# Kernel optimization log

Hardware: AMD Instinct MI355X
Metric: run time of the kernel (lower is better)

The kernel has to match this reference:

```python
import jax, jax.numpy as jnp
import numpy as np
from jax import lax

N, E, D, L = 10000, 320000, 128, 5
ATOM_V, BOND_V, WHID, CHID, P = 128, 16, 64, 20, 10
BN_EPS = 1e-5


def setup_inputs() -> dict:
    key = jax.random.key(0)
    it = iter(jax.random.split(key, 40))

    def nrm(shape, fan_in):
        return jax.random.normal(next(it), shape, jnp.float32) / np.sqrt(fan_in).astype(np.float32)

    return {
        "x_feat": jax.random.randint(next(it), (N, 2), 0, ATOM_V),
        "edge_index": jax.random.randint(next(it), (2, E), 0, N),
        "edge_attr": jax.random.randint(next(it), (E, 3), 0, BOND_V),
        "norm_edge_weight": jax.random.uniform(next(it), (E,), jnp.float32),
        "norm_self_loop": jax.random.uniform(next(it), (N,), jnp.float32),
        "atom_emb": nrm((2, ATOM_V, D), 1.0),
        "curv_w1": nrm((D, CHID), D), "curv_b1": jnp.zeros((CHID,), jnp.float32),
        "curv_w2": nrm((CHID, 1), CHID), "curv_b2": jnp.zeros((1,), jnp.float32),
        "fn_w1": nrm((D, CHID), D), "fn_b1": jnp.zeros((CHID,), jnp.float32),
        "fn_w2": nrm((CHID, 1), CHID), "fn_b2": jnp.zeros((1,), jnp.float32),
        "wm_w1": nrm((E, WHID), E), "wm_b1": jnp.zeros((WHID,), jnp.float32),
        "wm_w2": nrm((WHID, WHID), WHID), "wm_b2": jnp.zeros((WHID,), jnp.float32),
        "wm_w3": nrm((WHID, E), WHID), "wm_b3": jnp.zeros((E,), jnp.float32),
        "bond_emb": nrm((L, 3, BOND_V, D), 1.0),
        "conv_w1": nrm((L, D, D), D), "conv_b1": jnp.zeros((L, D), jnp.float32),
        "conv_bn_g": jnp.ones((L, D), jnp.float32), "conv_bn_b": jnp.zeros((L, D), jnp.float32),
        "conv_w2": nrm((L, D, D), D), "conv_b2": jnp.zeros((L, D), jnp.float32),
        "conv_eps": jnp.full((L,), 0.1, jnp.float32),
        "bn_g": jnp.ones((L, D), jnp.float32), "bn_b": jnp.zeros((L, D), jnp.float32),
        "batch": jnp.zeros((N,), jnp.int32),
    }


def _forward(x_feat, edge_index, edge_attr, norm_edge_weight, norm_self_loop,
             atom_emb, curv_w1, curv_b1, curv_w2, curv_b2,
             fn_w1, fn_b1, fn_w2, fn_b2,
             wm_w1, wm_b1, wm_w2, wm_b2, wm_w3, wm_b3,
             bond_emb, conv_w1, conv_b1, conv_bn_g, conv_bn_b, conv_w2, conv_b2,
             conv_eps, bn_g, bn_b):
    relu, sig = jax.nn.relu, jax.nn.sigmoid
    src, dst = edge_index[0], edge_index[1]

    # AtomEncoder: sum of per-column embeddings -> [N, D]
    x = atom_emb[0][x_feat[:, 0]] + atom_emb[1][x_feat[:, 1]]

    # CurvatureMLP: sigmoid(MLP(x)) -> kappa [N, 1]
    kappa = sig(relu(x @ curv_w1 + curv_b1) @ curv_w2 + curv_b2)

    # WeightMLP over 1-D edge-feature-sum vector (single sample of dim E)
    ea = edge_attr.sum(axis=1).astype(jnp.float32)  # [E]
    w = relu(ea @ wm_w1 + wm_b1)
    w = relu(w @ wm_w2 + wm_b2)
    weights = sig(w @ wm_w3 + wm_b3)  # [E]

    # curvature terms: scatter_add at SRC (as in original compute_gamma*)
    seg = lambda v: jax.ops.segment_sum(v, src, num_segments=N)
    f = sig(relu(x @ fn_w1 + fn_b1) @ fn_w2 + fn_b2)[:, 0]  # [N]
    fd = f[dst] - f[src]
    gamma = 0.5 * seg(weights * fd * fd)              # [N]
    delta_f = seg(weights * fd)                       # [N]
    delta_gamma = seg(weights * (gamma[dst] - gamma[src]))
    gfd = 0.5 * seg(weights * fd * (delta_f[dst] - delta_f[src]))
    gamma2 = 0.5 * delta_gamma - gfd                  # [N]
    # NOTE: kappa [N,1] * gamma [N] broadcasts to [N,N] (faithful to original)
    curv_loss = jnp.sum(relu(kappa * gamma - gamma2)) - jnp.sum(kappa)

    kap = kappa[:, 0]

    def bn(h, g, b):  # BatchNorm1d in training mode (batch stats, biased var)
        m = h.mean(axis=0)
        v = jnp.var(h, axis=0)
        return g * (h - m) * lax.rsqrt(v + BN_EPS) + b

    h_list = [x]
    for l in range(L):
        k = min(int(N * P * l / 100), 100)  # num vertices to suppress
        if k > 0:
            idx = lax.top_k(kap, k)[1]
            vm = jnp.ones(N, jnp.float32).at[idx].set(0.0)
            mew = jnp.where((vm[src] == 0) | (vm[dst] == 0), 1e-5, 1.0)
        else:
            mew = jnp.ones(E, jnp.float32)
        # BondEncoder for this layer
        ee = (bond_emb[l, 0][edge_attr[:, 0]]
              + bond_emb[l, 1][edge_attr[:, 1]]
              + bond_emb[l, 2][edge_attr[:, 2]])  # [E, D]
        # message: norm2 * norm * relu(x_j + edge_emb); aggregate add at dst
        msg = (mew * norm_edge_weight)[:, None] * relu(h_list[l][src] + ee)
        aggr = jax.ops.segment_sum(msg, dst, num_segments=N)
        h = conv_eps[l] * norm_self_loop[:, None] * h_list[l] + aggr
        # conv MLP: Linear -> BN -> ReLU -> Linear
        h = relu(bn(h @ conv_w1[l] + conv_b1[l], conv_bn_g[l], conv_bn_b[l])) @ conv_w2[l] + conv_b2[l]
        h = bn(h, bn_g[l], bn_b[l])
        if l < L - 1:  # dropout has ratio 0.0 -> no-op
            h = relu(h)
        h_list.append(h)

    node_rep = h_list[0]
    for h in h_list[1:]:
        node_rep = node_rep + h
    return node_rep, curv_loss


def reference(x_feat, edge_index, edge_attr, norm_edge_weight, norm_self_loop,
              atom_emb, curv_w1, curv_b1, curv_w2, curv_b2,
              fn_w1, fn_b1, fn_w2, fn_b2,
              wm_w1, wm_b1, wm_w2, wm_b2, wm_w3, wm_b3,
              bond_emb, conv_w1, conv_b1, conv_bn_g, conv_bn_b, conv_w2, conv_b2,
              conv_eps, bn_g, bn_b, batch):
    return _forward(x_feat, edge_index, edge_attr, norm_edge_weight, norm_self_loop,
                    atom_emb, curv_w1, curv_b1, curv_w2, curv_b2,
                    fn_w1, fn_b1, fn_w2, fn_b2,
                    wm_w1, wm_b1, wm_w2, wm_b2, wm_w3, wm_b3,
                    bond_emb, conv_w1, conv_b1, conv_bn_g, conv_bn_b, conv_w2, conv_b2,
                    conv_eps, bn_g, bn_b)
```

## Files before the change

### kernel.cpp

```cpp
#include <hip/hip_runtime.h>
#include <hip/hip_bf16.h>
#include <math.h>

#define N_NODES 10000
#define N_EDGES 320000
#define DIM     128
#define NLAYERS 5
#define CHIDN   20
#define BNEPS   1e-5f
#define TOPK    100

__device__ __forceinline__ float sigmoidf_(float x){ return 1.0f/(1.0f + expf(-x)); }

__global__ void k_init(int* counts, float* gamma, float* delta_f, float* dg, float* gfd,
                       double* wh_acc, double* kapsum, double* lossacc)
{
  int i = blockIdx.x*blockDim.x + threadIdx.x;
  int stride = gridDim.x*blockDim.x;
  for (int j=i; j<N_NODES; j+=stride){ counts[j]=0; gamma[j]=0.f; delta_f[j]=0.f; dg[j]=0.f; gfd[j]=0.f; }
  if (i < 64){ wh_acc[i]=0.0; kapsum[i]=0.0; lossacc[i]=0.0; }
}

__global__ __launch_bounds__(256) void k_node(
  const int* __restrict__ xf, const float* __restrict__ atom_emb,
  const float* __restrict__ cw1, const float* __restrict__ cb1,
  const float* __restrict__ cw2, const float* __restrict__ cb2,
  const float* __restrict__ fw1, const float* __restrict__ fb1,
  const float* __restrict__ fw2, const float* __restrict__ fb2,
  float* __restrict__ x_out, float* __restrict__ kap, float* __restrict__ fv,
  double* __restrict__ kapsum)
{
  __shared__ float scw1[DIM*CHIDN];
  __shared__ float sfw1[DIM*CHIDN];
  __shared__ float sx[4][DIM];
  __shared__ float sred[4][64];
  int tid = threadIdx.x;
  for (int i=tid;i<DIM*CHIDN;i+=256){ scw1[i]=cw1[i]; sfw1[i]=fw1[i]; }
  int wid = tid>>6, lane = tid&63;
  int n = blockIdx.x*4 + wid;
  const float* e0 = atom_emb;
  const float* e1 = atom_emb + 128*DIM;
  int f0 = xf[n*2+0], f1 = xf[n*2+1];
  float2 a = *(const float2*)(e0 + f0*DIM + lane*2);
  float2 b = *(const float2*)(e1 + f1*DIM + lane*2);
  float2 xv; xv.x = a.x+b.x; xv.y = a.y+b.y;
  *(float2*)(x_out + (size_t)n*DIM + lane*2) = xv;
  sx[wid][lane*2] = xv.x; sx[wid][lane*2+1] = xv.y;
  __syncthreads();
  if (lane < CHIDN) {
    float acc = cb1[lane];
    for (int d=0; d<DIM; ++d) acc = fmaf(sx[wid][d], scw1[d*CHIDN+lane], acc);
    sred[wid][lane] = fmaxf(acc, 0.f) * cw2[lane];
  } else if (lane >= 32 && lane < 32+CHIDN) {
    int hh = lane-32;
    float acc = fb1[hh];
    for (int d=0; d<DIM; ++d) acc = fmaf(sx[wid][d], sfw1[d*CHIDN+hh], acc);
    sred[wid][32+hh] = fmaxf(acc, 0.f) * fw2[hh];
  }
  __syncthreads();
  if (lane == 0) {
    float s = cb2[0];
    for (int h=0;h<CHIDN;++h) s += sred[wid][h];
    float kp = sigmoidf_(s);
    kap[n] = kp;
    sred[wid][62] = kp;
  } else if (lane == 1) {
    float s = fb2[0];
    for (int h=0;h<CHIDN;++h) s += sred[wid][32+h];
    fv[n] = sigmoidf_(s);
  }
  __syncthreads();
  if (tid == 0) {
    double ks = (double)sred[0][62] + (double)sred[1][62] + (double)sred[2][62] + (double)sred[3][62];
    atomicAdd(&kapsum[blockIdx.x & 63], ks);
  }
}

__global__ __launch_bounds__(256) void k_edge_pre(
  const int* __restrict__ ei, const int* __restrict__ eattr,
  const float* __restrict__ w1, int* __restrict__ counts, int* __restrict__ rank,
  double* __restrict__ wh_acc)
{
  __shared__ float part_[4][64];
  int tid = threadIdx.x;
  int wid = tid>>6, lane = tid&63;
  int bb = blockIdx.x*4 + wid;
  int e = bb*64 + lane;
  int a0=eattr[e*3], a1=eattr[e*3+1], a2=eattr[e*3+2];
  float ea = (float)(a0+a1+a2);
  int dst = ei[N_EDGES+e];
  rank[e] = atomicAdd(&counts[dst], 1);
  const float* wrow = w1 + (size_t)bb*64*64;
  float acc = 0.f;
  #pragma unroll 16
  for (int t=0;t<64;++t) {
    float eat = __shfl(ea, t);
    acc = fmaf(eat, wrow[t*64 + lane], acc);
  }
  part_[wid][lane] = acc;
  __syncthreads();
  if (tid < 64) {
    float s = part_[0][tid]+part_[1][tid]+part_[2][tid]+part_[3][tid];
    atomicAdd(&wh_acc[tid], (double)s);
  }
}

__global__ __launch_bounds__(1024) void k_topk_scan(
  const float* __restrict__ kap, int* __restrict__ mask,
  const int* __restrict__ counts, int* __restrict__ offs)
{
  __shared__ int sbuf[1024];
  __shared__ int hist[256];
  __shared__ unsigned s_prefix;
  __shared__ int s_krem;
  int tid = threadIdx.x;
  if (blockIdx.x == 0) {
    unsigned prefix = 0; int krem = TOPK;
    for (int pass=3; pass>=0; --pass) {
      if (tid<256) hist[tid]=0;
      __syncthreads();
      int shift = pass*8;
      unsigned hi_mask = (pass==3) ? 0u : (0xFFFFFFFFu << (shift+8));
      for (int i=tid;i<N_NODES;i+=1024) {
        unsigned b = __float_as_uint(kap[i]);
        if ((b & hi_mask) == (prefix & hi_mask))
          atomicAdd(&hist[(b>>shift)&255], 1);
      }
      __syncthreads();
      if (tid==0) {
        int c=0; int b=255;
        for (; b>0; --b){ int h=hist[b]; if (c+h >= krem) break; c+=h; }
        s_prefix = prefix | ((unsigned)b << shift);
        s_krem = krem - c;
      }
      __syncthreads();
      prefix = s_prefix; krem = s_krem;
      __syncthreads();
    }
    unsigned thr = prefix;
    const int per = 10;
    int base = tid*per;
    int cnt = 0;
    for (int i=base; i<base+per && i<N_NODES; ++i)
      if (__float_as_uint(kap[i])==thr) cnt++;
    sbuf[tid]=cnt; __syncthreads();
    for (int off=1; off<1024; off<<=1){
      int t = (tid>=off)? sbuf[tid-off] : 0;
      __syncthreads();
      sbuf[tid] += t;
      __syncthreads();
    }
    int taken = sbuf[tid] - cnt;
    for (int i=base; i<base+per && i<N_NODES; ++i) {
      unsigned b = __float_as_uint(kap[i]);
      int sel;
      if (b > thr) sel = 1;
      else if (b == thr) { sel = (taken < krem) ? 1 : 0; taken++; }
      else sel = 0;
      mask[i] = sel;
    }
  } else {
    int run = 0;
    for (int chunk=0; chunk<10; ++chunk) {
      int i = chunk*1024 + tid;
      int v = (i<N_NODES)? counts[i] : 0;
      sbuf[tid]=v; __syncthreads();
      for (int off=1; off<1024; off<<=1){
        int t = (tid>=off)? sbuf[tid-off]:0;
        __syncthreads();
        sbuf[tid]+=t;
        __syncthreads();
      }
      if (i<N_NODES) offs[i+1] = run + sbuf[tid];
      run += sbuf[1023];
      __syncthreads();
    }
    if (tid==0) offs[0]=0;
  }
}

__global__ __launch_bounds__(256) void k_weights(
  const double* __restrict__ wh_acc, const float* __restrict__ wb1,
  const float* __restrict__ wm2, const float* __restrict__ wb2,
  const float* __restrict__ w3, const float* __restrict__ wb3,
  float* __restrict__ weights)
{
  __shared__ float h1[64], h2[64];
  int tid = threadIdx.x;
  if (tid < 64) h1[tid] = fmaxf((float)wh_acc[tid] + wb1[tid], 0.f);
  __syncthreads();
  if (tid < 64) {
    float a = wb2[tid];
    for (int k=0;k<64;++k) a = fmaf(h1[k], wm2[k*64+tid], a);
    h2[tid] = fmaxf(a, 0.f);
  }
  __syncthreads();
  int e = blockIdx.x*256 + tid;
  float ws = wb3[e];
  #pragma unroll 16
  for (int h=0; h<64; ++h) ws = fmaf(h2[h], w3[(size_t)h*N_EDGES + e], ws);
  weights[e] = sigmoidf_(ws);
}

__global__ __launch_bounds__(256) void k_csr_fill(
  const int* __restrict__ ei, const int* __restrict__ eattr,
  const float* __restrict__ nev, const float* __restrict__ weights,
  const float* __restrict__ fv, const int* __restrict__ mask,
  const int* __restrict__ offs, const int* __restrict__ rank,
  float* __restrict__ gamma, float* __restrict__ delta_f,
  int4* __restrict__ csr)
{
  int e = blockIdx.x*256 + threadIdx.x;
  int s = ei[e], d = ei[N_EDGES + e];
  float wt = weights[e];
  float fd = fv[d] - fv[s];
  atomicAdd(&gamma[s], 0.5f*wt*fd*fd);
  atomicAdd(&delta_f[s], wt*fd);
  int a0 = eattr[e*3], a1 = eattr[e*3+1], a2 = eattr[e*3+2];
  float ew = nev[e];
  float mew = (mask[s] | mask[d]) ? 1e-5f : 1.0f;
  int4 rec;
  rec.x = s;
  rec.y = a0 | (a1<<8) | (a2<<16);
  rec.z = __float_as_int(ew);
  rec.w = __float_as_int(mew*ew);
  csr[offs[d] + rank[e]] = rec;
}

__global__ __launch_bounds__(256) void k_edge2(
  const int* __restrict__ ei, const float* __restrict__ weights,
  const float* __restrict__ fv, const float* __restrict__ gamma,
  const float* __restrict__ delta_f,
  float* __restrict__ dg, float* __restrict__ gfd)
{
  int e = blockIdx.x*256 + threadIdx.x;
  int s = ei[e], d = ei[N_EDGES+e];
  float wt = weights[e];
  atomicAdd(&dg[s], wt*(gamma[d]-gamma[s]));
  float fd = fv[d]-fv[s];
  atomicAdd(&gfd[s], wt*fd*(delta_f[d]-delta_f[s]));
}

__global__ __launch_bounds__(256) void k_loss(
  const float* __restrict__ kap, const float* __restrict__ gamma,
  const float* __restrict__ dg, const float* __restrict__ gfd,
  double* __restrict__ lossacc)
{
  __shared__ float skap[1250];
  __shared__ double dred[256];
  int tid = threadIdx.x;
  int i0 = blockIdx.y*1250;
  for (int i=tid;i<1250;i+=256) skap[i]=kap[i0+i];
  __syncthreads();
  int lane = tid & 63, part = tid >> 6;
  int j = blockIdx.x*64 + lane;
  float g=0.f, g2=0.f;
  bool valid = j < N_NODES;
  if (valid){ g = gamma[j]; g2 = 0.5f*(dg[j]-gfd[j]); }
  float sum = 0.f;
  if (valid) {
    int a = part*313, b = a+313; if (b>1250) b=1250;
    for (int i=a;i<b;++i) sum += fmaxf(fmaf(skap[i], g, -g2), 0.f);
  }
  dred[tid] = (double)sum;
  __syncthreads();
  for (int off=128; off>0; off>>=1){
    if (tid<off) dred[tid]+=dred[tid+off];
    __syncthreads();
  }
  if (tid==0) atomicAdd(&lossacc[blockIdx.x & 63], dred[0]);
}

__global__ void k_finalize(const double* __restrict__ lossacc, const double* __restrict__ kapsum,
                           float* __restrict__ out)
{
  if (threadIdx.x==0 && blockIdx.x==0){
    double acc = 0;
    for (int i=0;i<64;++i) acc += lossacc[i] - kapsum[i];
    out[N_NODES*DIM] = (float)acc;
  }
}

__global__ __launch_bounds__(256) void k_aggr(
  const float* __restrict__ hsrc, const double* __restrict__ statsPrev,
  const float* __restrict__ gPrev, const float* __restrict__ bPrev,
  const int4* __restrict__ csr, const int* __restrict__ offs,
  const float* __restrict__ bond_l, const float* __restrict__ nsl,
  const float* __restrict__ conv_eps, int l, int useW1,
  float* __restrict__ outP, double* __restrict__ stats_l)
{
  __shared__ float tab[3*16*DIM];
  __shared__ float s_sc[DIM], s_sh[DIM];
  int tid = threadIdx.x;
  for (int i=tid; i<3*16*DIM; i+=256) tab[i] = bond_l[i];
  bool bn = (statsPrev != nullptr);
  if (bn && tid < DIM) {
    double m = statsPrev[tid] * (1.0/N_NODES);
    double v = statsPrev[DIM+tid] * (1.0/N_NODES) - m*m;
    float inv = (float)(1.0/sqrt(v + (double)BNEPS));
    float sc = gPrev[tid]*inv;
    s_sc[tid]=sc; s_sh[tid]=bPrev[tid]-(float)m*sc;
  }
  if (blockIdx.x == 0) {
    for (int i=tid; i<512; i+=256) stats_l[i] = 0.0;
  }
  __syncthreads();
  int wid = tid>>6, lane = tid&63;
  int n = blockIdx.x*4 + wid;
  float scx=1.f, scy=1.f, shx=0.f, shy=0.f;
  if (bn){ scx=s_sc[lane*2]; scy=s_sc[lane*2+1]; shx=s_sh[lane*2]; shy=s_sh[lane*2+1]; }
  float2 h0 = *(const float2*)(hsrc + (size_t)n*DIM + lane*2);
  if (bn){ h0.x = fmaxf(fmaf(h0.x,scx,shx),0.f); h0.y = fmaxf(fmaf(h0.y,scy,shy),0.f); }
  float c = conv_eps[l] * nsl[n];
  float ax = c*h0.x, ay = c*h0.y;
  int beg = offs[n], end = offs[n+1];
  for (int j0=beg; j0<end; j0+=64) {
    int m = end - j0; if (m>64) m=64;
    int4 rec; rec.x=0; rec.y=0; rec.z=0; rec.w=0;
    float wsel = 0.f;
    if (lane < m) { rec = csr[j0+lane]; wsel = __int_as_float(useW1 ? rec.w : rec.z); }
    for (int t=0;t<m;++t) {
      int st = __shfl(rec.x, t);
      int a  = __shfl(rec.y, t);
      float wt = __shfl(wsel, t);
      float2 hs = *(const float2*)(hsrc + (size_t)st*DIM + lane*2);
      if (bn){ hs.x = fmaxf(fmaf(hs.x,scx,shx),0.f); hs.y = fmaxf(fmaf(hs.y,scy,shy),0.f); }
      int a0 = a&255, a1=(a>>8)&255, a2=(a>>16)&255;
      float2 e0 = *(const float2*)(tab + a0*DIM + lane*2);
      float2 e1 = *(const float2*)(tab + 16*DIM + a1*DIM + lane*2);
      float2 e2 = *(const float2*)(tab + 32*DIM + a2*DIM + lane*2);
      float vx = hs.x + e0.x + e1.x + e2.x;
      float vy = hs.y + e0.y + e1.y + e2.y;
      ax = fmaf(wt, fmaxf(vx,0.f), ax);
      ay = fmaf(wt, fmaxf(vy,0.f), ay);
    }
  }
  float2 o; o.x=ax; o.y=ay;
  *(float2*)(outP + (size_t)n*DIM + lane*2) = o;
}

__global__ __launch_bounds__(256) void k_gemm(
  const float* __restrict__ A, const float* __restrict__ W,
  const float* __restrict__ bias, float* __restrict__ Out,
  const double* __restrict__ statsIn, const float* __restrict__ gin, const float* __restrict__ bin,
  double* __restrict__ statsOut, int useBnIn)
{
  __shared__ __align__(16) float As[DIM*68];
  __shared__ __align__(16) float Ws[DIM*64];
  __shared__ float s_scale[DIM], s_shift[DIM];
  int tid = threadIdx.x;
  int r0 = blockIdx.x*64, c0 = blockIdx.y*64;
  if (useBnIn) {
    if (tid < DIM) {
      double m = statsIn[tid] * (1.0/N_NODES);
      double v = statsIn[DIM+tid] * (1.0/N_NODES) - m*m;
      float inv = (float)(1.0 / sqrt(v + (double)BNEPS));
      float sc = gin[tid]*inv;
      s_scale[tid] = sc;
      s_shift[tid] = bin[tid] - (float)m*sc;
    }
    __syncthreads();
  }
  for (int i=tid; i<2048; i+=256) {
    int k = i>>4, c4 = i&15;
    *(float4*)(&Ws[k*64 + c4*4]) = *(const float4*)(W + k*DIM + c0 + c4*4);
  }
  for (int i=tid; i<2048; i+=256) {
    int r = i&63, k4 = i>>6;
    int row = r0 + r;
    float4 v;
    if (row < N_NODES) v = *(const float4*)(A + (size_t)row*DIM + k4*4);
    else { v.x=0.f;v.y=0.f;v.z=0.f;v.w=0.f; }
    if (useBnIn) {
      int k = k4*4;
      v.x = fmaxf(fmaf(v.x, s_scale[k+0], s_shift[k+0]), 0.f);
      v.y = fmaxf(fmaf(v.y, s_scale[k+1], s_shift[k+1]), 0.f);
      v.z = fmaxf(fmaf(v.z, s_scale[k+2], s_shift[k+2]), 0.f);
      v.w = fmaxf(fmaf(v.w, s_scale[k+3], s_shift[k+3]), 0.f);
    }
    As[(k4*4+0)*68 + r] = v.x;
    As[(k4*4+1)*68 + r] = v.y;
    As[(k4*4+2)*68 + r] = v.z;
    As[(k4*4+3)*68 + r] = v.w;
  }
  __syncthreads();
  int tc = tid & 15, tr = tid >> 4;
  float acc[4][4];
  #pragma unroll
  for (int i=0;i<4;++i){ acc[i][0]=0.f; acc[i][1]=0.f; acc[i][2]=0.f; acc[i][3]=0.f; }
  #pragma unroll 4
  for (int k=0;k<DIM;++k) {
    float4 a4 = *(const float4*)(&As[k*68 + tr*4]);
    float4 w4 = *(const float4*)(&Ws[k*64 + tc*4]);
    acc[0][0]=fmaf(a4.x,w4.x,acc[0][0]); acc[0][1]=fmaf(a4.x,w4.y,acc[0][1]);
    acc[0][2]=fmaf(a4.x,w4.z,acc[0][2]); acc[0][3]=fmaf(a4.x,w4.w,acc[0][3]);
    acc[1][0]=fmaf(a4.y,w4.x,acc[1][0]); acc[1][1]=fmaf(a4.y,w4.y,acc[1][1]);
    acc[1][2]=fmaf(a4.y,w4.z,acc[1][2]); acc[1][3]=fmaf(a4.y,w4.w,acc[1][3]);
    acc[2][0]=fmaf(a4.z,w4.x,acc[2][0]); acc[2][1]=fmaf(a4.z,w4.y,acc[2][1]);
    acc[2][2]=fmaf(a4.z,w4.z,acc[2][2]); acc[2][3]=fmaf(a4.z,w4.w,acc[2][3]);
    acc[3][0]=fmaf(a4.w,w4.x,acc[3][0]); acc[3][1]=fmaf(a4.w,w4.y,acc[3][1]);
    acc[3][2]=fmaf(a4.w,w4.z,acc[3][2]); acc[3][3]=fmaf(a4.w,w4.w,acc[3][3]);
  }
  __syncthreads();
  float4 b4 = *(const float4*)(bias + c0 + tc*4);
  float ss[4]={0.f,0.f,0.f,0.f}, qq[4]={0.f,0.f,0.f,0.f};
  #pragma unroll
  for (int i=0;i<4;++i) {
    int row = r0 + tr*4 + i;
    if (row < N_NODES) {
      float o0=acc[i][0]+b4.x, o1=acc[i][1]+b4.y, o2=acc[i][2]+b4.z, o3=acc[i][3]+b4.w;
      float4 ov; ov.x=o0; ov.y=o1; ov.z=o2; ov.w=o3;
      *(float4*)(Out + (size_t)row*DIM + c0 + tc*4) = ov;
      ss[0]+=o0; ss[1]+=o1; ss[2]+=o2; ss[3]+=o3;
      qq[0]+=o0*o0; qq[1]+=o1*o1; qq[2]+=o2*o2; qq[3]+=o3*o3;
    }
  }
  float* rs = Ws;
  float* rq = Ws + 1024;
  #pragma unroll
  for (int j=0;j<4;++j){ rs[tr*64 + tc*4+j]=ss[j]; rq[tr*64 + tc*4+j]=qq[j]; }
  __syncthreads();
  if (tid < 64) {
    float s=0.f, q=0.f;
    #pragma unroll
    for (int t=0;t<16;++t){ s += rs[t*64+tid]; q += rq[t*64+tid]; }
    atomicAdd(&statsOut[c0+tid],       (double)s);
    atomicAdd(&statsOut[DIM+c0+tid],   (double)q);
  }
}

__global__ __launch_bounds__(256) void k_final(
  const float* __restrict__ x,
  const float* __restrict__ t0, const float* __restrict__ t1, const float* __restrict__ t2,
  const float* __restrict__ t3, const float* __restrict__ t4,
  const double* __restrict__ stats, const float* __restrict__ bn_g, const float* __restrict__ bn_b,
  float* __restrict__ out)
{
  __shared__ float sc[5][DIM], sh[5][DIM];
  int tid = threadIdx.x;
  if (tid < DIM) {
    for (int l=0;l<5;++l) {
      const double* st = stats + (size_t)l*512 + 256;
      double m = st[tid]*(1.0/N_NODES);
      double v = st[DIM+tid]*(1.0/N_NODES) - m*m;
      float inv = (float)(1.0/sqrt(v + (double)BNEPS));
      float s = bn_g[l*DIM+tid]*inv;
      sc[l][tid]=s; sh[l][tid]=bn_b[l*DIM+tid]-(float)m*s;
    }
  }
  __syncthreads();
  const float* ts[5] = {t0,t1,t2,t3,t4};
  int total = N_NODES*32;
  int stride = gridDim.x*256;
  for (int i = blockIdx.x*256 + tid; i < total; i += stride) {
    int c = (i & 31)*4;
    float4 a = ((const float4*)x)[i];
    #pragma unroll
    for (int l=0;l<5;++l) {
      float4 v = ((const float4*)ts[l])[i];
      v.x = fmaf(v.x, sc[l][c+0], sh[l][c+0]);
      v.y = fmaf(v.y, sc[l][c+1], sh[l][c+1]);
      v.z = fmaf(v.z, sc[l][c+2], sh[l][c+2]);
      v.w = fmaf(v.w, sc[l][c+3], sh[l][c+3]);
      if (l < 4) { v.x=fmaxf(v.x,0.f); v.y=fmaxf(v.y,0.f); v.z=fmaxf(v.z,0.f); v.w=fmaxf(v.w,0.f); }
      a.x+=v.x; a.y+=v.y; a.z+=v.z; a.w+=v.w;
    }
    ((float4*)out)[i] = a;
  }
}

extern "C" void kernel_launch(void* const* d_in, const int* in_sizes, int n_in,
                              void* d_out, int out_size, void* d_ws, size_t ws_size,
                              hipStream_t stream)
{
  const int*   x_feat   = (const int*)d_in[0];
  const int*   eidx     = (const int*)d_in[1];
  const int*   eattr    = (const int*)d_in[2];
  const float* nev      = (const float*)d_in[3];
  const float* nsl      = (const float*)d_in[4];
  const float* atom_emb = (const float*)d_in[5];
  const float* cw1 = (const float*)d_in[6];
  const float* cb1 = (const float*)d_in[7];
  const float* cw2 = (const float*)d_in[8];
  const float* cb2 = (const float*)d_in[9];
  const float* fw1 = (const float*)d_in[10];
  const float* fb1 = (const float*)d_in[11];
  const float* fw2 = (const float*)d_in[12];
  const float* fb2 = (const float*)d_in[13];
  const float* wm1 = (const float*)d_in[14];
  const float* wb1 = (const float*)d_in[15];
  const float* wm2 = (const float*)d_in[16];
  const float* wb2 = (const float*)d_in[17];
  const float* wm3 = (const float*)d_in[18];
  const float* wb3 = (const float*)d_in[19];
  const float* bond = (const float*)d_in[20];
  const float* conv_w1 = (const float*)d_in[21];
  const float* conv_b1 = (const float*)d_in[22];
  const float* conv_bn_g = (const float*)d_in[23];
  const float* conv_bn_b = (const float*)d_in[24];
  const float* conv_w2 = (const float*)d_in[25];
  const float* conv_b2 = (const float*)d_in[26];
  const float* conv_eps = (const float*)d_in[27];
  const float* bn_g = (const float*)d_in[28];
  const float* bn_b = (const float*)d_in[29];
  float* out = (float*)d_out;

  char* ws = (char*)d_ws;
  size_t off = 0;
  auto alloc = [&](size_t bytes)->char* {
    char* p = ws + off;
    off += (bytes + 255) & ~(size_t)255;
    return p;
  };
  float* hA       = (float*)alloc((size_t)N_NODES*DIM*4);
  float* bufP     = (float*)alloc((size_t)N_NODES*DIM*4);
  float* bufQ     = (float*)alloc((size_t)N_NODES*DIM*4);
  float* t2b[NLAYERS];
  for (int l=0;l<NLAYERS;++l) t2b[l] = (float*)alloc((size_t)N_NODES*DIM*4);
  int4*  csr      = (int4*)alloc((size_t)N_EDGES*16);
  float* weights  = (float*)alloc((size_t)N_EDGES*4);
  int*   rank     = (int*)alloc((size_t)N_EDGES*4);
  int*   counts   = (int*)alloc((size_t)N_NODES*4);
  int*   offs     = (int*)alloc((size_t)(N_NODES+1)*4);
  float* kap      = (float*)alloc((size_t)N_NODES*4);
  float* fv       = (float*)alloc((size_t)N_NODES*4);
  float* gamma    = (float*)alloc((size_t)N_NODES*4);
  float* delta_f  = (float*)alloc((size_t)N_NODES*4);
  float* dg       = (float*)alloc((size_t)N_NODES*4);
  float* gfd      = (float*)alloc((size_t)N_NODES*4);
  int*   mask     = (int*)alloc((size_t)N_NODES*4);
  double* wh_acc  = (double*)alloc(64*8);
  double* kapsum  = (double*)alloc(64*8);
  double* lossacc = (double*)alloc(64*8);
  double* stats   = (double*)alloc((size_t)NLAYERS*512*8);

  k_init<<<64, 256, 0, stream>>>(counts, gamma, delta_f, dg, gfd, wh_acc, kapsum, lossacc);
  k_node<<<N_NODES/4, 256, 0, stream>>>(x_feat, atom_emb, cw1,cb1,cw2,cb2, fw1,fb1,fw2,fb2,
                                        hA, kap, fv, kapsum);
  k_edge_pre<<<N_EDGES/256, 256, 0, stream>>>(eidx, eattr, wm1, counts, rank, wh_acc);
  k_topk_scan<<<2, 1024, 0, stream>>>(kap, mask, counts, offs);
  k_weights<<<N_EDGES/256, 256, 0, stream>>>(wh_acc, wb1, wm2, wb2, wm3, wb3, weights);
  k_csr_fill<<<N_EDGES/256, 256, 0, stream>>>(eidx, eattr, nev, weights, fv, mask, offs, rank,
                                              gamma, delta_f, csr);
  k_edge2<<<N_EDGES/256, 256, 0, stream>>>(eidx, weights, fv, gamma, delta_f, dg, gfd);
  k_loss<<<dim3((N_NODES+63)/64, 8), 256, 0, stream>>>(kap, gamma, dg, gfd, lossacc);
  k_finalize<<<1, 64, 0, stream>>>(lossacc, kapsum, out);

  for (int l=0; l<NLAYERS; ++l) {
    double* stats_l = stats + (size_t)l*512;
    const float* hsrc = (l==0) ? hA : t2b[l-1];
    const double* statsPrev = (l==0) ? nullptr : (stats + (size_t)(l-1)*512 + 256);
    const float* gPrev = bn_g + (size_t)(l>0?l-1:0)*DIM;
    const float* bPrev = bn_b + (size_t)(l>0?l-1:0)*DIM;
    k_aggr<<<N_NODES/4, 256, 0, stream>>>(hsrc, statsPrev, gPrev, bPrev, csr, offs,
                                          bond + (size_t)l*3*16*DIM, nsl, conv_eps, l,
                                          (l>0)?1:0, bufP, stats_l);
    k_gemm<<<dim3((N_NODES+63)/64, 2), 256, 0, stream>>>(bufP, conv_w1 + (size_t)l*DIM*DIM,
                conv_b1 + l*DIM, bufQ,
                (const double*)nullptr, (const float*)nullptr, (const float*)nullptr,
                stats_l, 0);
    k_gemm<<<dim3((N_NODES+63)/64, 2), 256, 0, stream>>>(bufQ, conv_w2 + (size_t)l*DIM*DIM,
                conv_b2 + l*DIM, t2b[l],
                stats_l, conv_bn_g + l*DIM, conv_bn_b + l*DIM,
                stats_l + 256, 1);
  }
  k_final<<<1024, 256, 0, stream>>>(hA, t2b[0], t2b[1], t2b[2], t2b[3], t2b[4],
                                    stats, bn_g, bn_b, out);
}
```

Baseline: 812.4 us.

## Fuse init, weights/CSR fill and loss finalize; vectorize edge_pre and stage CSR records

Moves buffer zeroing into k_node, merges k_weights with k_csr_fill, and folds the scalar loss finalize into an extra block of k_final that reduces per-block partials. The goal is to cut kernel launches and the double-precision atomics on hot slots. k_edge_pre now reads its weight rows as float4 and finishes with shuffle reductions. k_aggr stages each batch of CSR records in shared memory instead of broadcasting fields with shuffles. Summing kap partials in float changes rounding slightly, and the fused weights kernel carries more register pressure.

After: 724.3 us. 1.12x faster.

```diff
diff --git a/kernel.cpp b/kernel.cpp
--- a/kernel.cpp
+++ b/kernel.cpp
@@ -12,15 +12,6 @@
 
 __device__ __forceinline__ float sigmoidf_(float x){ return 1.0f/(1.0f + expf(-x)); }
 
-__global__ void k_init(int* counts, float* gamma, float* delta_f, float* dg, float* gfd,
-                       double* wh_acc, double* kapsum, double* lossacc)
-{
-  int i = blockIdx.x*blockDim.x + threadIdx.x;
-  int stride = gridDim.x*blockDim.x;
-  for (int j=i; j<N_NODES; j+=stride){ counts[j]=0; gamma[j]=0.f; delta_f[j]=0.f; dg[j]=0.f; gfd[j]=0.f; }
-  if (i < 64){ wh_acc[i]=0.0; kapsum[i]=0.0; lossacc[i]=0.0; }
-}
-
 __global__ __launch_bounds__(256) void k_node(
   const int* __restrict__ xf, const float* __restrict__ atom_emb,
   const float* __restrict__ cw1, const float* __restrict__ cb1,
@@ -28,13 +19,20 @@
   const float* __restrict__ fw1, const float* __restrict__ fb1,
   const float* __restrict__ fw2, const float* __restrict__ fb2,
   float* __restrict__ x_out, float* __restrict__ kap, float* __restrict__ fv,
-  double* __restrict__ kapsum)
+  float* __restrict__ kapparts,
+  int* __restrict__ counts, float* __restrict__ gamma, float* __restrict__ delta_f,
+  float* __restrict__ dg, float* __restrict__ gfd, double* __restrict__ wh_acc)
 {
   __shared__ float scw1[DIM*CHIDN];
   __shared__ float sfw1[DIM*CHIDN];
   __shared__ float sx[4][DIM];
   __shared__ float sred[4][64];
   int tid = threadIdx.x;
+  if (tid < 4) {
+    int n = blockIdx.x*4 + tid;
+    counts[n]=0; gamma[n]=0.f; delta_f[n]=0.f; dg[n]=0.f; gfd[n]=0.f;
+  }
+  if (blockIdx.x == 0 && tid < 64) wh_acc[tid] = 0.0;
   for (int i=tid;i<DIM*CHIDN;i+=256){ scw1[i]=cw1[i]; sfw1[i]=fw1[i]; }
   int wid = tid>>6, lane = tid&63;
   int n = blockIdx.x*4 + wid;
@@ -71,8 +69,7 @@
   }
   __syncthreads();
   if (tid == 0) {
-    double ks = (double)sred[0][62] + (double)sred[1][62] + (double)sred[2][62] + (double)sred[3][62];
-    atomicAdd(&kapsum[blockIdx.x & 63], ks);
+    kapparts[blockIdx.x] = sred[0][62] + sred[1][62] + sred[2][62] + sred[3][62];
   }
 }
 
@@ -90,14 +87,23 @@
   float ea = (float)(a0+a1+a2);
   int dst = ei[N_EDGES+e];
   rank[e] = atomicAdd(&counts[dst], 1);
-  const float* wrow = w1 + (size_t)bb*64*64;
-  float acc = 0.f;
-  #pragma unroll 16
-  for (int t=0;t<64;++t) {
-    float eat = __shfl(ea, t);
-    acc = fmaf(eat, wrow[t*64 + lane], acc);
-  }
-  part_[wid][lane] = acc;
+  const float4* wrow = (const float4*)(w1 + (size_t)bb*64*64);
+  int rsub = lane>>4, c4 = lane&15;
+  float4 acc; acc.x=0.f; acc.y=0.f; acc.z=0.f; acc.w=0.f;
+  #pragma unroll
+  for (int i=0;i<16;++i) {
+    float4 v = wrow[(i*4+rsub)*16 + c4];
+    float eat = __shfl(ea, i*4+rsub);
+    acc.x = fmaf(eat, v.x, acc.x);
+    acc.y = fmaf(eat, v.y, acc.y);
+    acc.z = fmaf(eat, v.z, acc.z);
+    acc.w = fmaf(eat, v.w, acc.w);
+  }
+  acc.x += __shfl_xor(acc.x, 16); acc.y += __shfl_xor(acc.y, 16);
+  acc.z += __shfl_xor(acc.z, 16); acc.w += __shfl_xor(acc.w, 16);
+  acc.x += __shfl_xor(acc.x, 32); acc.y += __shfl_xor(acc.y, 32);
+  acc.z += __shfl_xor(acc.z, 32); acc.w += __shfl_xor(acc.w, 32);
+  if (lane < 16) ((float4*)part_[wid])[c4] = acc;
   __syncthreads();
   if (tid < 64) {
     float s = part_[0][tid]+part_[1][tid]+part_[2][tid]+part_[3][tid];
@@ -179,11 +185,16 @@
   }
 }
 
-__global__ __launch_bounds__(256) void k_weights(
+__global__ __launch_bounds__(256) void k_weights_csr(
   const double* __restrict__ wh_acc, const float* __restrict__ wb1,
   const float* __restrict__ wm2, const float* __restrict__ wb2,
   const float* __restrict__ w3, const float* __restrict__ wb3,
-  float* __restrict__ weights)
+  const int* __restrict__ ei, const int* __restrict__ eattr,
+  const float* __restrict__ nev, const float* __restrict__ fv,
+  const int* __restrict__ mask, const int* __restrict__ offs,
+  const int* __restrict__ rank,
+  float* __restrict__ weights, float* __restrict__ gamma, float* __restrict__ delta_f,
+  int4* __restrict__ csr)
 {
   __shared__ float h1[64], h2[64];
   int tid = threadIdx.x;
@@ -199,20 +210,9 @@
   float ws = wb3[e];
   #pragma unroll 16
   for (int h=0; h<64; ++h) ws = fmaf(h2[h], w3[(size_t)h*N_EDGES + e], ws);
-  weights[e] = sigmoidf_(ws);
-}
-
-__global__ __launch_bounds__(256) void k_csr_fill(
-  const int* __restrict__ ei, const int* __restrict__ eattr,
-  const float* __restrict__ nev, const float* __restrict__ weights,
-  const float* __restrict__ fv, const int* __restrict__ mask,
-  const int* __restrict__ offs, const int* __restrict__ rank,
-  float* __restrict__ gamma, float* __restrict__ delta_f,
-  int4* __restrict__ csr)
-{
-  int e = blockIdx.x*256 + threadIdx.x;
+  float wt = sigmoidf_(ws);
+  weights[e] = wt;
   int s = ei[e], d = ei[N_EDGES + e];
-  float wt = weights[e];
   float fd = fv[d] - fv[s];
   atomicAdd(&gamma[s], 0.5f*wt*fd*fd);
   atomicAdd(&delta_f[s], wt*fd);
@@ -244,7 +244,7 @@
 __global__ __launch_bounds__(256) void k_loss(
   const float* __restrict__ kap, const float* __restrict__ gamma,
   const float* __restrict__ dg, const float* __restrict__ gfd,
-  double* __restrict__ lossacc)
+  double* __restrict__ lossparts)
 {
   __shared__ float skap[1250];
   __shared__ double dred[256];
@@ -268,17 +268,7 @@
     if (tid<off) dred[tid]+=dred[tid+off];
     __syncthreads();
   }
-  if (tid==0) atomicAdd(&lossacc[blockIdx.x & 63], dred[0]);
-}
-
-__global__ void k_finalize(const double* __restrict__ lossacc, const double* __restrict__ kapsum,
-                           float* __restrict__ out)
-{
-  if (threadIdx.x==0 && blockIdx.x==0){
-    double acc = 0;
-    for (int i=0;i<64;++i) acc += lossacc[i] - kapsum[i];
-    out[N_NODES*DIM] = (float)acc;
-  }
+  if (tid==0) lossparts[blockIdx.y*157 + blockIdx.x] = dred[0];
 }
 
 __global__ __launch_bounds__(256) void k_aggr(
@@ -291,6 +281,7 @@
 {
   __shared__ float tab[3*16*DIM];
   __shared__ float s_sc[DIM], s_sh[DIM];
+  __shared__ int4 srec[4][64];
   int tid = threadIdx.x;
   for (int i=tid; i<3*16*DIM; i+=256) tab[i] = bond_l[i];
   bool bn = (statsPrev != nullptr);
@@ -316,16 +307,14 @@
   int beg = offs[n], end = offs[n+1];
   for (int j0=beg; j0<end; j0+=64) {
     int m = end - j0; if (m>64) m=64;
-    int4 rec; rec.x=0; rec.y=0; rec.z=0; rec.w=0;
-    float wsel = 0.f;
-    if (lane < m) { rec = csr[j0+lane]; wsel = __int_as_float(useW1 ? rec.w : rec.z); }
+    if (lane < m) srec[wid][lane] = csr[j0+lane];
+    #pragma unroll 4
     for (int t=0;t<m;++t) {
-      int st = __shfl(rec.x, t);
-      int a  = __shfl(rec.y, t);
-      float wt = __shfl(wsel, t);
-      float2 hs = *(const float2*)(hsrc + (size_t)st*DIM + lane*2);
+      int4 r = srec[wid][t];
+      float wt = __int_as_float(useW1 ? r.w : r.z);
+      float2 hs = *(const float2*)(hsrc + (size_t)r.x*DIM + lane*2);
       if (bn){ hs.x = fmaxf(fmaf(hs.x,scx,shx),0.f); hs.y = fmaxf(fmaf(hs.y,scy,shy),0.f); }
-      int a0 = a&255, a1=(a>>8)&255, a2=(a>>16)&255;
+      int a0 = r.y&255, a1=(r.y>>8)&255, a2=(r.y>>16)&255;
       float2 e0 = *(const float2*)(tab + a0*DIM + lane*2);
       float2 e1 = *(const float2*)(tab + 16*DIM + a1*DIM + lane*2);
       float2 e2 = *(const float2*)(tab + 32*DIM + a2*DIM + lane*2);
@@ -434,10 +423,25 @@
   const float* __restrict__ t0, const float* __restrict__ t1, const float* __restrict__ t2,
   const float* __restrict__ t3, const float* __restrict__ t4,
   const double* __restrict__ stats, const float* __restrict__ bn_g, const float* __restrict__ bn_b,
+  const double* __restrict__ lossparts, const float* __restrict__ kapparts,
   float* __restrict__ out)
 {
+  int tid = threadIdx.x;
+  if (blockIdx.x == 0) {
+    __shared__ double red[256];
+    double acc = 0.0;
+    for (int i=tid; i<1256; i+=256) acc += lossparts[i];
+    for (int i=tid; i<2500; i+=256) acc -= (double)kapparts[i];
+    red[tid] = acc;
+    __syncthreads();
+    for (int off=128; off>0; off>>=1){
+      if (tid<off) red[tid]+=red[tid+off];
+      __syncthreads();
+    }
+    if (tid==0) out[N_NODES*DIM] = (float)red[0];
+    return;
+  }
   __shared__ float sc[5][DIM], sh[5][DIM];
-  int tid = threadIdx.x;
   if (tid < DIM) {
     for (int l=0;l<5;++l) {
       const double* st = stats + (size_t)l*512 + 256;
@@ -451,8 +455,8 @@
   __syncthreads();
   const float* ts[5] = {t0,t1,t2,t3,t4};
   int total = N_NODES*32;
-  int stride = gridDim.x*256;
-  for (int i = blockIdx.x*256 + tid; i < total; i += stride) {
+  int stride = (gridDim.x-1)*256;
+  for (int i = (blockIdx.x-1)*256 + tid; i < total; i += stride) {
     int c = (i & 31)*4;
     float4 a = ((const float4*)x)[i];
     #pragma unroll
@@ -530,21 +534,20 @@
   float* gfd      = (float*)alloc((size_t)N_NODES*4);
   int*   mask     = (int*)alloc((size_t)N_NODES*4);
   double* wh_acc  = (double*)alloc(64*8);
-  double* kapsum  = (double*)alloc(64*8);
-  double* lossacc = (double*)alloc(64*8);
+  float* kapparts = (float*)alloc(2500*4);
+  double* lossparts = (double*)alloc(1256*8);
   double* stats   = (double*)alloc((size_t)NLAYERS*512*8);
 
-  k_init<<<64, 256, 0, stream>>>(counts, gamma, delta_f, dg, gfd, wh_acc, kapsum, lossacc);
   k_node<<<N_NODES/4, 256, 0, stream>>>(x_feat, atom_emb, cw1,cb1,cw2,cb2, fw1,fb1,fw2,fb2,
-                                        hA, kap, fv, kapsum);
+                                        hA, kap, fv, kapparts,
+                                        counts, gamma, delta_f, dg, gfd, wh_acc);
   k_edge_pre<<<N_EDGES/256, 256, 0, stream>>>(eidx, eattr, wm1, counts, rank, wh_acc);
   k_topk_scan<<<2, 1024, 0, stream>>>(kap, mask, counts, offs);
-  k_weights<<<N_EDGES/256, 256, 0, stream>>>(wh_acc, wb1, wm2, wb2, wm3, wb3, weights);
-  k_csr_fill<<<N_EDGES/256, 256, 0, stream>>>(eidx, eattr, nev, weights, fv, mask, offs, rank,
-                                              gamma, delta_f, csr);
+  k_weights_csr<<<N_EDGES/256, 256, 0, stream>>>(wh_acc, wb1, wm2, wb2, wm3, wb3,
+                                                 eidx, eattr, nev, fv, mask, offs, rank,
+                                                 weights, gamma, delta_f, csr);
   k_edge2<<<N_EDGES/256, 256, 0, stream>>>(eidx, weights, fv, gamma, delta_f, dg, gfd);
-  k_loss<<<dim3((N_NODES+63)/64, 8), 256, 0, stream>>>(kap, gamma, dg, gfd, lossacc);
-  k_finalize<<<1, 64, 0, stream>>>(lossacc, kapsum, out);
+  k_loss<<<dim3((N_NODES+63)/64, 8), 256, 0, stream>>>(kap, gamma, dg, gfd, lossparts);
 
   for (int l=0; l<NLAYERS; ++l) {
     double* stats_l = stats + (size_t)l*512;
@@ -564,6 +567,6 @@
                 stats_l, conv_bn_g + l*DIM, conv_bn_b + l*DIM,
                 stats_l + 256, 1);
   }
-  k_final<<<1024, 256, 0, stream>>>(hA, t2b[0], t2b[1], t2b[2], t2b[3], t2b[4],
-                                    stats, bn_g, bn_b, out);
-}
+  k_final<<<1025, 256, 0, stream>>>(hA, t2b[0], t2b[1], t2b[2], t2b[3], t2b[4],
+                                    stats, bn_g, bn_b, lossparts, kapparts, out);
+}
```
